# Optimization experiments

Measured on AMD Instinct MI355X. Metric: run time of the kernel, lower is better.

## Reference

```python
import jax, jax.numpy as jnp
import numpy as np
from jax import lax

EPS = 1e-5

# int4 fake-quant (Brevitas-style, per-tensor float scale)
# signed act: [-8, 7]; unsigned act: [0, 15]; weight narrow-range: [-7, 7]

def ste_round(x):
    # straight-through round (matches Brevitas STE; forward math == round)
    return x + lax.stop_gradient(jnp.round(x) - x)

def fq(x, s, lo, hi):
    return jnp.clip(ste_round(x / s), lo, hi) * s

def qw(w):
    # Int4WeightQuant: per-tensor scale from max-abs stats, narrow range [-7,7]
    s = jnp.max(jnp.abs(w)) / 7.0
    return jnp.clip(ste_round(w / s), -7.0, 7.0) * s

def conv(x, w, pad):
    return lax.conv_general_dilated(x, w, (1, 1), pad,
                                    dimension_numbers=('NCHW', 'OIHW', 'NCHW'))

def maxpool2(x):
    return lax.reduce_window(x, -jnp.inf, lax.max, (1, 1, 2, 2), (1, 1, 2, 2), 'VALID')

def bn_apply(x, bn):
    g, b, m, v = bn[0], bn[1], bn[2], bn[3]
    inv = g / jnp.sqrt(v + EPS)
    return x * inv[None, :, None, None] + (b - m * inv)[None, :, None, None]

def block(x, w, bn, s_in, s_relu, pool):
    x = fq(x, s_in, -8.0, 7.0)          # conv input_quant (signed int4)
    x = conv(x, qw(w), 'SAME')          # 3x3 quant conv, no bias
    x = bn_apply(x, bn)                 # BatchNorm (eval, running stats)
    x = jax.nn.relu(x)
    x = fq(x, s_relu, 0.0, 15.0)        # QuantReLU (unsigned int4)
    return maxpool2(x) if pool else x

def _forward(x, ws, b9, bns, scales):
    x = fq(x, scales[0], -8.0, 7.0)     # QuantIdentity (signed int4)
    for i in range(8):
        x = block(x, ws[i], bns[i], scales[1 + i], scales[10 + i], pool=(i < 4))
    x = fq(x, scales[9], -8.0, 7.0)     # head input_quant
    x = conv(x, qw(ws[8]), 'VALID') + b9[None, :, None, None]  # 1x1 head with bias
    return x


def setup_inputs() -> dict:
    key = jax.random.key(0)
    ks = jax.random.split(key, 32)
    B, H, W = 16, 320, 640
    x = jax.random.normal(ks[0], (B, 3, H, W), dtype=jnp.float32)
    wshapes = [(16, 3, 3, 3), (32, 16, 3, 3), (64, 32, 3, 3)] + [(64, 64, 3, 3)] * 5 + [(36, 64, 1, 1)]
    inp = {'x': x}
    for i, sh in enumerate(wshapes):
        inp[f'w{i+1}'] = 0.05 * jax.random.normal(ks[1 + i], sh, dtype=jnp.float32)
    inp['b9'] = 0.01 * jax.random.normal(ks[10], (36,), dtype=jnp.float32)
    chans = [16, 32, 64, 64, 64, 64, 64, 64]
    for i, c in enumerate(chans):
        k1, k2, k3, k4 = jax.random.split(ks[11 + i], 4)
        g = 0.75 + 0.5 * jax.random.uniform(k1, (c,), dtype=jnp.float32)
        b = 0.1 * jax.random.normal(k2, (c,), dtype=jnp.float32)
        m = 0.1 * jax.random.normal(k3, (c,), dtype=jnp.float32)
        v = 0.5 + 0.5 * jax.random.uniform(k4, (c,), dtype=jnp.float32)
        inp[f'bn{i+1}'] = jnp.stack([g, b, m, v])  # (4, C)
    inp['scales'] = 0.02 + 0.1 * jax.random.uniform(ks[30], (18,), dtype=jnp.float32)
    return inp


def reference(x, w1, w2, w3, w4, w5, w6, w7, w8, w9, b9,
              bn1, bn2, bn3, bn4, bn5, bn6, bn7, bn8, scales):
    ws = [w1, w2, w3, w4, w5, w6, w7, w8, w9]
    bns = [bn1, bn2, bn3, bn4, bn5, bn6, bn7, bn8]
    return _forward(x, ws, b9, bns, scales)
```

## Files before the change

### kernel.cpp

```cpp
#include <hip/hip_runtime.h>
#include <stdint.h>

#define EPSV 1e-5f

typedef int v4i __attribute__((ext_vector_type(4)));

__device__ __forceinline__ v4i mfma16(v4i a, v4i b, v4i c) {
    return __builtin_amdgcn_mfma_i32_16x16x64_i8(a, b, c, 0, 0, 0);
}

__device__ __forceinline__ int dot4(int a, int b, int c) {
#if __has_builtin(__builtin_amdgcn_sdot4)
    return __builtin_amdgcn_sdot4(a, b, c, false);
#else
    int r = c;
#pragma unroll
    for (int i = 0; i < 4; ++i)
        r += ((int)(int8_t)(a >> (8 * i))) * ((int)(int8_t)(b >> (8 * i)));
    return r;
#endif
}

__device__ __forceinline__ int8_t q_epi(int s, float fscale, float inv, float beta,
                                        float s_relu, float s_next)
{
#pragma clang fp contract(off)
    float y = (float)s * fscale;
    y = y * inv;
    y = y + beta;
    float r = rintf(y / s_relu);
    r = fminf(fmaxf(r, 0.f), 15.f);
    float v = r * s_relu;
    float r2 = rintf(v / s_next);
    r2 = fminf(fmaxf(r2, -8.f), 7.f);
    return (int8_t)(int)r2;
}

struct WPtrs { const float* w[9]; int n[9]; };

__global__ __launch_bounds__(256) void k_wmax(WPtrs a, unsigned* __restrict__ smax)
{
    const int t = blockIdx.y;
    const int n = a.n[t];
    const float* w = a.w[t];
    float m = 0.f;
    for (int i = blockIdx.x * 256 + threadIdx.x; i < n; i += 16 * 256)
        m = fmaxf(m, fabsf(w[i]));
#pragma unroll
    for (int off = 32; off > 0; off >>= 1) m = fmaxf(m, __shfl_down(m, off));
    __shared__ float red[4];
    if ((threadIdx.x & 63) == 0) red[threadIdx.x >> 6] = m;
    __syncthreads();
    if (threadIdx.x == 0) {
        m = fmaxf(fmaxf(red[0], red[1]), fmaxf(red[2], red[3]));
        atomicMax(smax + t, __float_as_uint(m));
    }
}

struct PackArgs {
    const float* w[9];
    const float* bn[8];
    const float* x;
    const float* scales;
    const unsigned* smax;
    int* qw;
    float* bnp;
    int* a0;
};

#define NB_B    207
#define NB_HEAD 3
#define NB_BN   2
#define NB_INQ  12800

__global__ __launch_bounds__(256) void k_pack(PackArgs a)
{
#pragma clang fp contract(off)
    const int blk = blockIdx.x;
    if (blk < NB_B) {
        const int u = blk * 256 + threadIdx.x;
        const int bcum[9] = {0, 256, 1792, 6912, 16128, 25344, 34560, 43776, 52992};
        const int CIGA[8] = {1, 4, 8, 16, 16, 16, 16, 16};
        const int COA[8]  = {16, 32, 64, 64, 64, 64, 64, 64};
        const int NTA[8]  = {1, 2, 4, 4, 4, 4, 4, 4};
        const int CINA[8] = {3, 16, 32, 64, 64, 64, 64, 64};
        int L = 0;
        while (u >= bcum[L + 1]) ++L;
        const int rem = u - bcum[L];
        const int d = rem & 3;
        const int lane = (rem >> 2) & 63;
        const int gnt = rem >> 8;
        const int NT = NTA[L];
        const int nt = gnt % NT;
        const int g = gnt / NT;
        const int CIG = CIGA[L], CIN = CINA[L], CO = COA[L];
        const int TG = 16 / CIG;
        const int n = nt * 16 + (lane & 15);
        const float s = __uint_as_float(a.smax[L]) / 7.0f;
        const float* w = a.w[L];
        unsigned dw = 0;
        for (int jb = 0; jb < 4; ++jb) {
            const int k = 16 * (lane >> 4) + 4 * d + jb;
            const int tap = g * TG + k / (4 * CIG);
            const int ci = k % (4 * CIG);
            int qv = 0;
            if (tap < 9 && ci < CIN && n < CO) {
                float rr = rintf(w[(n * CIN + ci) * 9 + tap] / s);
                rr = fminf(fmaxf(rr, -7.f), 7.f);
                qv = (int)rr;
            }
            dw |= ((unsigned)(qv & 0xff)) << (8 * jb);
        }
        a.qw[u] = (int)dw;
    } else if (blk < NB_B + NB_HEAD) {
        const int u = (blk - NB_B) * 256 + threadIdx.x;
        if (u >= 576) return;
        const int co = u % 36;
        const int cig = u / 36;
        const float s = __uint_as_float(a.smax[8]) / 7.0f;
        const float* w = a.w[8];
        unsigned dw = 0;
        for (int jb = 0; jb < 4; ++jb) {
            const int ci = 4 * cig + jb;
            float rr = rintf(w[co * 64 + ci] / s);
            rr = fminf(fmaxf(rr, -7.f), 7.f);
            dw |= ((unsigned)(((int)rr) & 0xff)) << (8 * jb);
        }
        a.qw[52992 + u] = (int)dw;
    } else if (blk < NB_B + NB_HEAD + NB_BN) {
        const int id = (blk - NB_B - NB_HEAD) * 256 + threadIdx.x;
        if (id >= 512) return;
        const int l = id >> 6, c = id & 63;
        const int C[8] = {16, 32, 64, 64, 64, 64, 64, 64};
        if (c < C[l]) {
            const float* bn = a.bn[l];
            const int Cl = C[l];
            float g = bn[c], b = bn[Cl + c], m = bn[2 * Cl + c], v = bn[3 * Cl + c];
            float inv = g / sqrtf(v + EPSV);
            float mi = m * inv;
            a.bnp[l * 128 + c] = inv;
            a.bnp[l * 128 + 64 + c] = b - mi;
        }
    } else {
        const int p = (blk - NB_B - NB_HEAD - NB_BN) * 256 + threadIdx.x;
        const int HW = 320 * 640;
        const int b = p / HW;
        const int rest = p - b * HW;
        const float s0 = a.scales[0], s1 = a.scales[1];
        unsigned dw = 0;
#pragma unroll
        for (int ci = 0; ci < 3; ++ci) {
            float xv = a.x[(b * 3 + ci) * HW + rest];
            float r = rintf(xv / s0);
            r = fminf(fmaxf(r, -8.f), 7.f);
            float v = r * s0;
            float r2 = rintf(v / s1);
            r2 = fminf(fmaxf(r2, -8.f), 7.f);
            dw |= ((unsigned)(((int)r2) & 0xff)) << (8 * ci);
        }
        a.a0[p] = (int)dw;
    }
}

template <int CIG, int CO, bool POOL, int H, int W, int XL, int NROWS>
__global__ __launch_bounds__(256) void k_mconv(
    const int8_t* __restrict__ in, int8_t* __restrict__ out,
    const int* __restrict__ bfrag, const float* __restrict__ scales,
    const unsigned* __restrict__ smax, const float* __restrict__ bnp,
    int layer, int sin_idx, int srelu_idx, int snext_idx)
{
    constexpr int NT = CO / 16;
    constexpr int TG = 16 / CIG;
    constexpr int NG = (9 + TG - 1) / TG;
    constexpr int WPR = POOL ? 1 : 2;
    constexpr int NTW = POOL ? NT : NT / 2;
    constexpr int OPW = POOL ? 4 : 16;
    constexpr int S = POOL ? 2 : 1;
    constexpr int TLH = S * NROWS + 2;
    constexpr int TLW = S * OPW * XL + 2;
    constexpr int TILE_DW = TLH * TLW * CIG;
    constexpr bool BLDS = (CIG >= 8);
    constexpr int BDW = NG * NT * 256;
    constexpr int Ho = POOL ? H / 2 : H;
    constexpr int Wo = POOL ? W / 2 : W;
    static_assert(WPR * NROWS == 4, "4 waves per block");
    static_assert(POOL || CIG == 16, "nonpool path assumes CIG=16");

    __shared__ int tile[TILE_DW];
    __shared__ int bsh[BLDS ? BDW : 1];
    __shared__ float bnl[128];

    const int b = blockIdx.z;
    const int py0 = blockIdx.y * NROWS;
    const int px0 = blockIdx.x * (OPW * XL);
    const int ty0 = S * py0 - 1;
    const int tx0 = S * px0 - 1;
    const int* gin = (const int*)in;

    for (int i = threadIdx.x; i < TILE_DW; i += 256) {
        const int cig = i % CIG;
        const int rest = i / CIG;
        const int lx = rest % TLW;
        const int ly = rest / TLW;
        const int gy = ty0 + ly, gx = tx0 + lx;
        int v = 0;
        if ((unsigned)gy < (unsigned)H && (unsigned)gx < (unsigned)W)
            v = gin[((b * H + gy) * W + gx) * CIG + cig];
        tile[i] = v;
    }
    if (BLDS)
        for (int i = threadIdx.x; i < BDW; i += 256) bsh[i] = bfrag[i];
    if (threadIdx.x < 128) bnl[threadIdx.x] = bnp[layer * 128 + threadIdx.x];

    const int lane = threadIdx.x & 63;
    const int wv = threadIdx.x >> 6;
    v4i breg[BLDS ? 1 : NG * NT];
    if (!BLDS) {
#pragma unroll
        for (int i = 0; i < NG * NT; ++i)
            breg[i] = *(const v4i*)&bfrag[(i * 64 + lane) * 4];
    }
    __syncthreads();

    const int q = lane >> 4;
    const int m = lane & 15;

    const float swv = __uint_as_float(smax[layer]) / 7.0f;
    const float fscale = scales[sin_idx] * swv;
    const float s_relu = scales[srelu_idx];
    const float s_next = scales[snext_idx];

    int lyb, lxb0, wrow, nt0;
    if (POOL) {
        const int px_sub = m >> 2;
        const int op = m & 3;
        wrow = wv;
        nt0 = 0;
        lyb = 2 * wrow + (op >> 1);
        lxb0 = 2 * px_sub + (op & 1);
    } else {
        wrow = wv >> 1;
        nt0 = (wv & 1) * NTW;
        lyb = wrow;
        lxb0 = m;
    }

    for (int xs = 0; xs < XL; ++xs) {
        v4i acc[NTW];
#pragma unroll
        for (int j = 0; j < NTW; ++j) acc[j] = (v4i){0, 0, 0, 0};

#pragma unroll
        for (int g = 0; g < NG; ++g) {
            v4i af;
            if constexpr (CIG == 16) {
                const int ky = (g * 11) >> 5;
                const int kx = g - 3 * ky;
                int addr;
                if (POOL) addr = ((lyb + ky) * TLW + (8 * xs + lxb0 + kx)) * 16 + 4 * q;
                else      addr = ((lyb + ky) * TLW + (lxb0 + kx)) * 16 + 4 * q;
                af = *(const v4i*)&tile[addr];
            } else if constexpr (CIG == 8) {
                int t = 2 * g + (q >> 1); t = min(t, 8);
                const int ky = (t * 11) >> 5;
                const int kx = t - 3 * ky;
                const int addr = ((lyb + ky) * TLW + (8 * xs + lxb0 + kx)) * 8 + 4 * (q & 1);
                af = *(const v4i*)&tile[addr];
            } else if constexpr (CIG == 4) {
                int t = 4 * g + q; t = min(t, 8);
                const int ky = (t * 11) >> 5;
                const int kx = t - 3 * ky;
                const int addr = ((lyb + ky) * TLW + (8 * xs + lxb0 + kx)) * 4;
                af = *(const v4i*)&tile[addr];
            } else {
#pragma unroll
                for (int d = 0; d < 4; ++d) {
                    int t = 4 * q + d; t = min(t, 8);
                    const int ky = (t * 11) >> 5;
                    const int kx = t - 3 * ky;
                    af[d] = tile[(lyb + ky) * TLW + (8 * xs + lxb0 + kx)];
                }
            }
#pragma unroll
            for (int j = 0; j < NTW; ++j) {
                const int nt = nt0 + j;
                v4i bf;
                if (BLDS) bf = *(const v4i*)&bsh[((g * NT + nt) * 64 + lane) * 4];
                else      bf = breg[g * NT + nt];
                acc[j] = mfma16(af, bf, acc[j]);
            }
        }

        if (POOL) {
            const int py = py0 + wrow;
            const int px = px0 + 4 * xs + q;
            int8_t* po = out + ((size_t)((b * Ho + py) * Wo + px)) * CO + m;
#pragma unroll
            for (int j = 0; j < NTW; ++j) {
                const int co = j * 16 + m;
                const int s = max(max(acc[j][0], acc[j][1]), max(acc[j][2], acc[j][3]));
                po[j * 16] = q_epi(s, fscale, bnl[co], bnl[64 + co], s_relu, s_next);
            }
        } else {
            const int py = py0 + wrow;
#pragma unroll
            for (int j = 0; j < NTW; ++j) {
                const int co = (nt0 + j) * 16 + m;
                const float inv = bnl[co], beta = bnl[64 + co];
#pragma unroll
                for (int r = 0; r < 4; ++r) {
                    const int px = px0 + 4 * q + r;
                    if (px < Wo)
                        out[((size_t)((b * Ho + py) * Wo + px)) * CO + co] =
                            q_epi(acc[j][r], fscale, inv, beta, s_relu, s_next);
                }
            }
        }
    }
}

__global__ __launch_bounds__(256) void k_head(
    const int8_t* __restrict__ in,
    float* __restrict__ out,
    const int* __restrict__ wq,
    const float* __restrict__ scales,
    const unsigned* __restrict__ smax,
    const float* __restrict__ b9)
{
#pragma clang fp contract(off)
    __shared__ int wl[576];
    for (int i = threadIdx.x; i < 576; i += 256) wl[i] = wq[i];
    __syncthreads();
    const int px = blockIdx.x * 256 + threadIdx.x;
    const int b = blockIdx.y;
    if (px >= 800) return;
    const int* ip = (const int*)in + (size_t)(b * 800 + px) * 16;
    int p[16];
#pragma unroll
    for (int c4 = 0; c4 < 4; ++c4) *(int4*)&p[4 * c4] = *(const int4*)&ip[4 * c4];
    const float fs = scales[9] * (__uint_as_float(smax[8]) / 7.0f);
    for (int co = 0; co < 36; ++co) {
        int acc = 0;
#pragma unroll
        for (int cig = 0; cig < 16; ++cig) acc = dot4(p[cig], wl[cig * 36 + co], acc);
        float y = (float)acc * fs;
        out[(size_t)(b * 36 + co) * 800 + px] = y + b9[co];
    }
}

extern "C" void kernel_launch(void* const* d_in, const int* in_sizes, int n_in,
                              void* d_out, int out_size, void* d_ws, size_t ws_size,
                              hipStream_t stream)
{
    const float* x = (const float*)d_in[0];
    const float* w[9];
    for (int i = 0; i < 9; i++) w[i] = (const float*)d_in[1 + i];
    const float* b9 = (const float*)d_in[10];
    const float* bn[8];
    for (int i = 0; i < 8; i++) bn[i] = (const float*)d_in[11 + i];
    const float* scales = (const float*)d_in[19];

    int8_t* base = (int8_t*)d_ws;
    int8_t* bufA = base;
    int8_t* bufB = base + 13107200;
    int*     qw  = (int*)(base + 26214400);
    unsigned* smax = (unsigned*)(base + 26429440);
    float*   bnp = (float*)(base + 26429952);

    static const int wn[9] = {432, 4608, 18432, 36864, 36864, 36864, 36864, 36864, 2304};
    static const int bo[8] = {0, 256, 1792, 6912, 16128, 25344, 34560, 43776};

    hipMemsetAsync(smax, 0, 9 * sizeof(unsigned), stream);

    WPtrs wp;
    for (int i = 0; i < 9; i++) { wp.w[i] = w[i]; wp.n[i] = wn[i]; }
    k_wmax<<<dim3(16, 9), 256, 0, stream>>>(wp, smax);

    PackArgs pa;
    for (int i = 0; i < 9; i++) pa.w[i] = w[i];
    for (int i = 0; i < 8; i++) pa.bn[i] = bn[i];
    pa.x = x; pa.scales = scales; pa.smax = smax;
    pa.qw = qw; pa.bnp = bnp; pa.a0 = (int*)bufA;
    k_pack<<<NB_B + NB_HEAD + NB_BN + NB_INQ, 256, 0, stream>>>(pa);

    k_mconv<1, 16, true, 320, 640, 8, 4><<<dim3(10, 40, 16), 256, 0, stream>>>(
        bufA, bufB, qw + bo[0], scales, smax, bnp, 0, 1, 10, 2);
    k_mconv<4, 32, true, 160, 320, 4, 4><<<dim3(10, 20, 16), 256, 0, stream>>>(
        bufB, bufA, qw + bo[1], scales, smax, bnp, 1, 2, 11, 3);
    k_mconv<8, 64, true, 80, 160, 2, 4><<<dim3(10, 10, 16), 256, 0, stream>>>(
        bufA, bufB, qw + bo[2], scales, smax, bnp, 2, 3, 12, 4);
    k_mconv<16, 64, true, 40, 80, 1, 4><<<dim3(10, 5, 16), 256, 0, stream>>>(
        bufB, bufA, qw + bo[3], scales, smax, bnp, 3, 4, 13, 5);
    k_mconv<16, 64, false, 20, 40, 1, 2><<<dim3(3, 10, 16), 256, 0, stream>>>(
        bufA, bufB, qw + bo[4], scales, smax, bnp, 4, 5, 14, 6);
    k_mconv<16, 64, false, 20, 40, 1, 2><<<dim3(3, 10, 16), 256, 0, stream>>>(
        bufB, bufA, qw + bo[5], scales, smax, bnp, 5, 6, 15, 7);
    k_mconv<16, 64, false, 20, 40, 1, 2><<<dim3(3, 10, 16), 256, 0, stream>>>(
        bufA, bufB, qw + bo[6], scales, smax, bnp, 6, 7, 16, 8);
    k_mconv<16, 64, false, 20, 40, 1, 2><<<dim3(3, 10, 16), 256, 0, stream>>>(
        bufB, bufA, qw + bo[7], scales, smax, bnp, 7, 8, 17, 9);

    k_head<<<dim3(4, 16), 256, 0, stream>>>(
        bufA, (float*)d_out, qw + 52992, scales, smax, b9);

    (void)in_sizes; (void)n_in; (void)out_size; (void)ws_size;
}
```

Measured before the change: 221.2 us.

## Fuse input quantization into first conv and 1x1 head into last conv

Removes the separate input-quant pass that wrote a packed int8 copy of x. A new first-layer conv kernel now quantizes the float input straight into its shared tile. The final 3x3 layer keeps its quantized codes in shared memory and runs the 1x1 head with an MFMA, which removes the k_head launch and the buffer round trip. B-fragments for larger layers are no longer staged in LDS and are read from global memory instead. This trades LDS staging for cache reads and recomputes input quantization on halo pixels.

```diff
diff --git a/kernel.cpp b/kernel.cpp
--- a/kernel.cpp
+++ b/kernel.cpp
@@ -7,18 +7,6 @@
 
 __device__ __forceinline__ v4i mfma16(v4i a, v4i b, v4i c) {
     return __builtin_amdgcn_mfma_i32_16x16x64_i8(a, b, c, 0, 0, 0);
-}
-
-__device__ __forceinline__ int dot4(int a, int b, int c) {
-#if __has_builtin(__builtin_amdgcn_sdot4)
-    return __builtin_amdgcn_sdot4(a, b, c, false);
-#else
-    int r = c;
-#pragma unroll
-    for (int i = 0; i < 4; ++i)
-        r += ((int)(int8_t)(a >> (8 * i))) * ((int)(int8_t)(b >> (8 * i)));
-    return r;
-#endif
 }
 
 __device__ __forceinline__ int8_t q_epi(int s, float fscale, float inv, float beta,
@@ -60,18 +48,14 @@
 struct PackArgs {
     const float* w[9];
     const float* bn[8];
-    const float* x;
-    const float* scales;
     const unsigned* smax;
     int* qw;
     float* bnp;
-    int* a0;
 };
 
 #define NB_B    207
 #define NB_HEAD 3
 #define NB_BN   2
-#define NB_INQ  12800
 
 __global__ __launch_bounds__(256) void k_pack(PackArgs a)
 {
@@ -113,21 +97,26 @@
         }
         a.qw[u] = (int)dw;
     } else if (blk < NB_B + NB_HEAD) {
-        const int u = (blk - NB_B) * 256 + threadIdx.x;
-        if (u >= 576) return;
-        const int co = u % 36;
-        const int cig = u / 36;
+        const int uh = (blk - NB_B) * 256 + threadIdx.x;
+        const int d = uh & 3;
+        const int lane = (uh >> 2) & 63;
+        const int nt = uh >> 8;
+        const int n = nt * 16 + (lane & 15);
         const float s = __uint_as_float(a.smax[8]) / 7.0f;
         const float* w = a.w[8];
         unsigned dw = 0;
         for (int jb = 0; jb < 4; ++jb) {
-            const int ci = 4 * cig + jb;
-            float rr = rintf(w[co * 64 + ci] / s);
-            rr = fminf(fmaxf(rr, -7.f), 7.f);
-            dw |= ((unsigned)(((int)rr) & 0xff)) << (8 * jb);
-        }
-        a.qw[52992 + u] = (int)dw;
-    } else if (blk < NB_B + NB_HEAD + NB_BN) {
+            const int ci = 16 * (lane >> 4) + 4 * d + jb;
+            int qv = 0;
+            if (n < 36) {
+                float rr = rintf(w[n * 64 + ci] / s);
+                rr = fminf(fmaxf(rr, -7.f), 7.f);
+                qv = (int)rr;
+            }
+            dw |= ((unsigned)(qv & 0xff)) << (8 * jb);
+        }
+        a.qw[52992 + uh] = (int)dw;
+    } else {
         const int id = (blk - NB_B - NB_HEAD) * 256 + threadIdx.x;
         if (id >= 512) return;
         const int l = id >> 6, c = id & 63;
@@ -141,33 +130,91 @@
             a.bnp[l * 128 + c] = inv;
             a.bnp[l * 128 + 64 + c] = b - mi;
         }
-    } else {
-        const int p = (blk - NB_B - NB_HEAD - NB_BN) * 256 + threadIdx.x;
-        const int HW = 320 * 640;
-        const int b = p / HW;
-        const int rest = p - b * HW;
-        const float s0 = a.scales[0], s1 = a.scales[1];
-        unsigned dw = 0;
-#pragma unroll
-        for (int ci = 0; ci < 3; ++ci) {
-            float xv = a.x[(b * 3 + ci) * HW + rest];
-            float r = rintf(xv / s0);
-            r = fminf(fmaxf(r, -8.f), 7.f);
-            float v = r * s0;
-            float r2 = rintf(v / s1);
-            r2 = fminf(fmaxf(r2, -8.f), 7.f);
-            dw |= ((unsigned)(((int)r2) & 0xff)) << (8 * ci);
-        }
-        a.a0[p] = (int)dw;
-    }
-}
-
-template <int CIG, int CO, bool POOL, int H, int W, int XL, int NROWS>
+    }
+}
+
+__global__ __launch_bounds__(256) void k_conv0(
+    const float* __restrict__ x, int8_t* __restrict__ out,
+    const int* __restrict__ bfrag, const float* __restrict__ scales,
+    const unsigned* __restrict__ smax, const float* __restrict__ bnp)
+{
+#pragma clang fp contract(off)
+    __shared__ int tile[660];
+    __shared__ float bnl[128];
+
+    const int b = blockIdx.z;
+    const int py0 = blockIdx.y * 4;
+    const int px0 = blockIdx.x * 32;
+    const int ty0 = 2 * py0 - 1;
+    const int tx0 = 2 * px0 - 1;
+    const float s0 = scales[0], s1 = scales[1];
+
+    for (int i = threadIdx.x; i < 660; i += 256) {
+        const int ly = i / 66;
+        const int lx = i - ly * 66;
+        const int gy = ty0 + ly, gx = tx0 + lx;
+        int v = 0;
+        if ((unsigned)gy < 320u && (unsigned)gx < 640u) {
+#pragma unroll
+            for (int ci = 0; ci < 3; ++ci) {
+                float xv = x[((size_t)(b * 3 + ci) * 320 + gy) * 640 + gx];
+                float r = rintf(xv / s0);
+                r = fminf(fmaxf(r, -8.f), 7.f);
+                float vv = r * s0;
+                float r2 = rintf(vv / s1);
+                r2 = fminf(fmaxf(r2, -8.f), 7.f);
+                v |= ((int)r2 & 0xff) << (8 * ci);
+            }
+        }
+        tile[i] = v;
+    }
+    if (threadIdx.x < 128) bnl[threadIdx.x] = bnp[threadIdx.x];
+
+    const int lane = threadIdx.x & 63;
+    const int wv = threadIdx.x >> 6;
+    const v4i bfv = *(const v4i*)&bfrag[lane * 4];
+    __syncthreads();
+
+    const int q = lane >> 4;
+    const int m = lane & 15;
+    const int px_sub = m >> 2;
+    const int op = m & 3;
+    const int lyb = 2 * wv + (op >> 1);
+    const int lxb0 = 2 * px_sub + (op & 1);
+
+    const float sw = __uint_as_float(smax[0]) / 7.0f;
+    const float fscale = scales[1] * sw;
+    const float s_relu = scales[10];
+    const float s_next = scales[2];
+    const float inv = bnl[m];
+    const float beta = bnl[64 + m];
+    const int py = py0 + wv;
+
+    for (int xs = 0; xs < 8; ++xs) {
+        v4i af;
+#pragma unroll
+        for (int d = 0; d < 4; ++d) {
+            int t = 4 * q + d; t = min(t, 8);
+            const int ky = (t * 11) >> 5;
+            const int kx = t - 3 * ky;
+            af[d] = tile[(lyb + ky) * 66 + 8 * xs + lxb0 + kx];
+        }
+        v4i acc = mfma16(af, bfv, (v4i){0, 0, 0, 0});
+        const int px = px0 + 4 * xs + q;
+        const int s = max(max(acc[0], acc[1]), max(acc[2], acc[3]));
+        out[((size_t)((b * 160 + py) * 320 + px)) * 16 + m] =
+            q_epi(s, fscale, inv, beta, s_relu, s_next);
+    }
+}
+
+template <int CIG, int CO, bool POOL, int H, int W, int XL, int NROWS, bool FUSED>
 __global__ __launch_bounds__(256) void k_mconv(
     const int8_t* __restrict__ in, int8_t* __restrict__ out,
     const int* __restrict__ bfrag, const float* __restrict__ scales,
     const unsigned* __restrict__ smax, const float* __restrict__ bnp,
-    int layer, int sin_idx, int srelu_idx, int snext_idx)
+    int layer, int sin_idx, int srelu_idx, int snext_idx,
+    const int* __restrict__ hfrag, const float* __restrict__ b9,
+    float* __restrict__ dout)
 {
     constexpr int NT = CO / 16;
     constexpr int TG = 16 / CIG;
@@ -179,16 +226,16 @@
     constexpr int TLH = S * NROWS + 2;
     constexpr int TLW = S * OPW * XL + 2;
     constexpr int TILE_DW = TLH * TLW * CIG;
-    constexpr bool BLDS = (CIG >= 8);
-    constexpr int BDW = NG * NT * 256;
+    constexpr bool PRELOAD = (NG * NT <= 8);
     constexpr int Ho = POOL ? H / 2 : H;
     constexpr int Wo = POOL ? W / 2 : W;
     static_assert(WPR * NROWS == 4, "4 waves per block");
     static_assert(POOL || CIG == 16, "nonpool path assumes CIG=16");
+    static_assert(!FUSED || (!POOL && XL == 1 && NROWS == 2), "fused head shape");
 
     __shared__ int tile[TILE_DW];
-    __shared__ int bsh[BLDS ? BDW : 1];
     __shared__ float bnl[128];
+    __shared__ int code_dw[FUSED ? 512 : 1];
 
     const int b = blockIdx.z;
     const int py0 = blockIdx.y * NROWS;
@@ -198,7 +245,7 @@
     const int* gin = (const int*)in;
 
     for (int i = threadIdx.x; i < TILE_DW; i += 256) {
-        const int cig = i % CIG;
+        const int cig = i & (CIG - 1);
         const int rest = i / CIG;
         const int lx = rest % TLW;
         const int ly = rest / TLW;
@@ -208,14 +255,12 @@
             v = gin[((b * H + gy) * W + gx) * CIG + cig];
         tile[i] = v;
     }
-    if (BLDS)
-        for (int i = threadIdx.x; i < BDW; i += 256) bsh[i] = bfrag[i];
     if (threadIdx.x < 128) bnl[threadIdx.x] = bnp[layer * 128 + threadIdx.x];
 
     const int lane = threadIdx.x & 63;
     const int wv = threadIdx.x >> 6;
-    v4i breg[BLDS ? 1 : NG * NT];
-    if (!BLDS) {
+    v4i breg[PRELOAD ? NG * NT : 1];
+    if constexpr (PRELOAD) {
 #pragma unroll
         for (int i = 0; i < NG * NT; ++i)
             breg[i] = *(const v4i*)&bfrag[(i * 64 + lane) * 4];
@@ -283,10 +328,9 @@
             }
 #pragma unroll
             for (int j = 0; j < NTW; ++j) {
-                const int nt = nt0 + j;
                 v4i bf;
-                if (BLDS) bf = *(const v4i*)&bsh[((g * NT + nt) * 64 + lane) * 4];
-                else      bf = breg[g * NT + nt];
+                if constexpr (PRELOAD) bf = breg[g * NT + nt0 + j];
+                else bf = *(const v4i*)&bfrag[((g * NT + nt0 + j) * 64 + lane) * 4];
                 acc[j] = mfma16(af, bf, acc[j]);
             }
         }
@@ -310,41 +354,43 @@
 #pragma unroll
                 for (int r = 0; r < 4; ++r) {
                     const int px = px0 + 4 * q + r;
-                    if (px < Wo)
-                        out[((size_t)((b * Ho + py) * Wo + px)) * CO + co] =
-                            q_epi(acc[j][r], fscale, inv, beta, s_relu, s_next);
+                    const int8_t cb = q_epi(acc[j][r], fscale, inv, beta, s_relu, s_next);
+                    if constexpr (FUSED) {
+                        ((int8_t*)code_dw)[(wrow * 16 + 4 * q + r) * 64 + co] = cb;
+                    } else {
+                        if (px < Wo)
+                            out[((size_t)((b * Ho + py) * Wo + px)) * CO + co] = cb;
+                    }
                 }
             }
         }
     }
-}
-
-__global__ __launch_bounds__(256) void k_head(
-    const int8_t* __restrict__ in,
-    float* __restrict__ out,
-    const int* __restrict__ wq,
-    const float* __restrict__ scales,
-    const unsigned* __restrict__ smax,
-    const float* __restrict__ b9)
-{
+
+    if constexpr (FUSED) {
+        __syncthreads();
+        if (wv < 2) {
 #pragma clang fp contract(off)
-    __shared__ int wl[576];
-    for (int i = threadIdx.x; i < 576; i += 256) wl[i] = wq[i];
-    __syncthreads();
-    const int px = blockIdx.x * 256 + threadIdx.x;
-    const int b = blockIdx.y;
-    if (px >= 800) return;
-    const int* ip = (const int*)in + (size_t)(b * 800 + px) * 16;
-    int p[16];
-#pragma unroll
-    for (int c4 = 0; c4 < 4; ++c4) *(int4*)&p[4 * c4] = *(const int4*)&ip[4 * c4];
-    const float fs = scales[9] * (__uint_as_float(smax[8]) / 7.0f);
-    for (int co = 0; co < 36; ++co) {
-        int acc = 0;
-#pragma unroll
-        for (int cig = 0; cig < 16; ++cig) acc = dot4(p[cig], wl[cig * 36 + co], acc);
-        float y = (float)acc * fs;
-        out[(size_t)(b * 36 + co) * 800 + px] = y + b9[co];
+            const v4i ha = *(const v4i*)&code_dw[(wv * 16 + m) * 16 + 4 * q];
+            const float fs = scales[9] * (__uint_as_float(smax[8]) / 7.0f);
+            const int py2 = py0 + wv;
+#pragma unroll
+            for (int nt = 0; nt < 3; ++nt) {
+                const v4i hb = *(const v4i*)&hfrag[(nt * 64 + lane) * 4];
+                const v4i hacc = mfma16(ha, hb, (v4i){0, 0, 0, 0});
+                const int co = nt * 16 + m;
+                if (co < 36) {
+                    const float bias = b9[co];
+#pragma unroll
+                    for (int r = 0; r < 4; ++r) {
+                        const int px = px0 + 4 * q + r;
+                        if (px < 40) {
+                            float y = (float)hacc[r] * fs;
+                            dout[((size_t)(b * 36 + co)) * 800 + py2 * 40 + px] = y + bias;
+                        }
+                    }
+                }
+            }
+        }
     }
 }
 
@@ -379,29 +425,27 @@
     PackArgs pa;
     for (int i = 0; i < 9; i++) pa.w[i] = w[i];
     for (int i = 0; i < 8; i++) pa.bn[i] = bn[i];
-    pa.x = x; pa.scales = scales; pa.smax = smax;
-    pa.qw = qw; pa.bnp = bnp; pa.a0 = (int*)bufA;
-    k_pack<<<NB_B + NB_HEAD + NB_BN + NB_INQ, 256, 0, stream>>>(pa);
-
-    k_mconv<1, 16, true, 320, 640, 8, 4><<<dim3(10, 40, 16), 256, 0, stream>>>(
-        bufA, bufB, qw + bo[0], scales, smax, bnp, 0, 1, 10, 2);
-    k_mconv<4, 32, true, 160, 320, 4, 4><<<dim3(10, 20, 16), 256, 0, stream>>>(
-        bufB, bufA, qw + bo[1], scales, smax, bnp, 1, 2, 11, 3);
-    k_mconv<8, 64, true, 80, 160, 2, 4><<<dim3(10, 10, 16), 256, 0, stream>>>(
-        bufA, bufB, qw + bo[2], scales, smax, bnp, 2, 3, 12, 4);
-    k_mconv<16, 64, true, 40, 80, 1, 4><<<dim3(10, 5, 16), 256, 0, stream>>>(
-        bufB, bufA, qw + bo[3], scales, smax, bnp, 3, 4, 13, 5);
-    k_mconv<16, 64, false, 20, 40, 1, 2><<<dim3(3, 10, 16), 256, 0, stream>>>(
-        bufA, bufB, qw + bo[4], scales, smax, bnp, 4, 5, 14, 6);
-    k_mconv<16, 64, false, 20, 40, 1, 2><<<dim3(3, 10, 16), 256, 0, stream>>>(
-        bufB, bufA, qw + bo[5], scales, smax, bnp, 5, 6, 15, 7);
-    k_mconv<16, 64, false, 20, 40, 1, 2><<<dim3(3, 10, 16), 256, 0, stream>>>(
-        bufA, bufB, qw + bo[6], scales, smax, bnp, 6, 7, 16, 8);
-    k_mconv<16, 64, false, 20, 40, 1, 2><<<dim3(3, 10, 16), 256, 0, stream>>>(
-        bufB, bufA, qw + bo[7], scales, smax, bnp, 7, 8, 17, 9);
-
-    k_head<<<dim3(4, 16), 256, 0, stream>>>(
-        bufA, (float*)d_out, qw + 52992, scales, smax, b9);
+    pa.smax = smax; pa.qw = qw; pa.bnp = bnp;
+    k_pack<<<NB_B + NB_HEAD + NB_BN, 256, 0, stream>>>(pa);
+
+    k_conv0<<<dim3(10, 40, 16), 256, 0, stream>>>(
+        x, bufB, qw + bo[0], scales, smax, bnp);
+
+    k_mconv<4, 32, true, 160, 320, 4, 4, false><<<dim3(10, 20, 16), 256, 0, stream>>>(
+        bufB, bufA, qw + bo[1], scales, smax, bnp, 1, 2, 11, 3, nullptr, nullptr, nullptr);
+    k_mconv<8, 64, true, 80, 160, 2, 4, false><<<dim3(10, 10, 16), 256, 0, stream>>>(
+        bufA, bufB, qw + bo[2], scales, smax, bnp, 2, 3, 12, 4, nullptr, nullptr, nullptr);
+    k_mconv<16, 64, true, 40, 80, 1, 4, false><<<dim3(10, 5, 16), 256, 0, stream>>>(
+        bufB, bufA, qw + bo[3], scales, smax, bnp, 3, 4, 13, 5, nullptr, nullptr, nullptr);
+    k_mconv<16, 64, false, 20, 40, 1, 2, false><<<dim3(3, 10, 16), 256, 0, stream>>>(
+        bufA, bufB, qw + bo[4], scales, smax, bnp, 4, 5, 14, 6, nullptr, nullptr, nullptr);
+    k_mconv<16, 64, false, 20, 40, 1, 2, false><<<dim3(3, 10, 16), 256, 0, stream>>>(
+        bufB, bufA, qw + bo[5], scales, smax, bnp, 5, 6, 15, 7, nullptr, nullptr, nullptr);
+    k_mconv<16, 64, false, 20, 40, 1, 2, false><<<dim3(3, 10, 16), 256, 0, stream>>>(
+        bufA, bufB, qw + bo[6], scales, smax, bnp, 6, 7, 16, 8, nullptr, nullptr, nullptr);
+    k_mconv<16, 64, false, 20, 40, 1, 2, true><<<dim3(3, 10, 16), 256, 0, stream>>>(
+        bufB, bufA, qw + bo[7], scales, smax, bnp, 7, 8, 17, 9,
+        qw + 52992, b9, (float*)d_out);
 
     (void)in_sizes; (void)n_in; (void)out_size; (void)ws_size;
 }
```

After: 216.6 us. 1.02x faster.
